# Kernel tuning notes

Measured on AMD Instinct MI355X. Metric: run time of the kernel, lower is better.

Reference implementation:

```python
import jax, jax.numpy as jnp
import numpy as np

GRID_SHAPE = (32, 32)
TEMPERATURE = 1.0


def setup_inputs() -> dict:
    key = jax.random.key(0)
    k1, k2 = jax.random.split(key)
    x = jax.random.normal(k1, (16384, 1024), dtype=jnp.float32)
    som_weights = jax.random.normal(k2, (*GRID_SHAPE, 1024), dtype=jnp.float32) * 0.05
    return {"x": x, "som_weights": som_weights}


def reference(x, som_weights):
    # x: [B, D]; som_weights: [G1, G2, D]
    B, D = x.shape
    g1, g2 = GRID_SHAPE
    w_flat = som_weights.reshape(g1 * g2, D)  # [N, D]
    x_sq = jnp.sum(x * x, axis=-1, keepdims=True)          # [B, 1]
    w_sq = jnp.sum(w_flat * w_flat, axis=-1)[None, :]       # [1, N]
    d2 = x_sq - 2.0 * (x @ w_flat.T) + w_sq                 # [B, N]
    logits = (-d2 / TEMPERATURE).reshape(B, g1, g2)         # [B, G1, G2]
    # per-dimension softmax along each spatial axis, combined multiplicatively
    s1 = jax.nn.softmax(logits, axis=1)
    s2 = jax.nn.softmax(logits, axis=2)
    combined = s1 * s2
    combined = combined / (jnp.sum(combined, axis=(1, 2), keepdims=True) + 1e-8)
    # soft reconstruction: weighted sum over grid of codebook vectors
    recon = jnp.einsum('bn,nd->bd', combined.reshape(B, g1 * g2), w_flat)
    return recon
```

## Files before the change

### kernel.cpp

```cpp
#include <hip/hip_runtime.h>
#include <hip/hip_bf16.h>

static constexpr int BATCH = 16384;
static constexpr int DIM   = 1024;
static constexpr int NN    = 1024;
static constexpr int G     = 32;

typedef _Float16 half8  __attribute__((ext_vector_type(8)));
typedef _Float16 half4v __attribute__((ext_vector_type(4)));
typedef float    f32x4  __attribute__((ext_vector_type(4)));

__global__ __launch_bounds__(256) void transpose_w_kernel(const float* __restrict__ W,
                                                          _Float16* __restrict__ Wh,
                                                          _Float16* __restrict__ WTh) {
    __shared__ _Float16 tile[64][72];
    const int t  = threadIdx.x;
    const int n0 = (blockIdx.x & 15) * 64;
    const int d0 = (blockIdx.x >> 4) * 64;
#pragma unroll
    for (int p = 0; p < 4; ++p) {
        int n = n0 + p * 16 + (t >> 4);
        int d = d0 + (t & 15) * 4;
        float4 v = *(const float4*)(W + (size_t)n * DIM + d);
        half4v h;
        h[0] = (_Float16)v.x; h[1] = (_Float16)v.y;
        h[2] = (_Float16)v.z; h[3] = (_Float16)v.w;
        *(half4v*)(Wh + (size_t)n * DIM + d) = h;
#pragma unroll
        for (int k = 0; k < 4; ++k)
            tile[(t & 15) * 4 + k][p * 16 + (t >> 4)] = h[k];
    }
    __syncthreads();
#pragma unroll
    for (int p = 0; p < 4; ++p) {
        int dp = p * 16 + (t >> 4);
        int nc = (t & 15) * 4;
        half4v hv = *(const half4v*)&tile[dp][nc];
        *(half4v*)(WTh + (size_t)(d0 + dp) * NN + n0 + nc) = hv;
    }
}

__global__ __launch_bounds__(256) void wsq_kernel(const float* __restrict__ W,
                                                  float* __restrict__ wsq) {
    const int n = blockIdx.x;
    const int t = threadIdx.x;
    float4 v = *(const float4*)(W + (size_t)n * DIM + 4 * t);
    float ss = v.x * v.x + v.y * v.y + v.z * v.z + v.w * v.w;
#pragma unroll
    for (int o = 32; o > 0; o >>= 1) ss += __shfl_xor(ss, o, 64);
    __shared__ float red[4];
    if ((t & 63) == 0) red[t >> 6] = ss;
    __syncthreads();
    if (t == 0) wsq[n] = red[0] + red[1] + red[2] + red[3];
}

template <typename AT, int EPI>
__global__ __launch_bounds__(256) void gemm_bt_kernel(const AT* __restrict__ A,
                                                      const _Float16* __restrict__ B,
                                                      float* __restrict__ C,
                                                      const float* __restrict__ wsq,
                                                      int M, int N, int K) {
    constexpr bool AF32 = sizeof(AT) == 4;
    __shared__ __align__(16) AT       As[128 * 64];
    __shared__ __align__(16) _Float16 Bs[128 * 64];

    const int t  = threadIdx.x;
    const int l  = t & 63;
    const int wv = t >> 6;

    const int NT  = N >> 7;
    const int MT  = M >> 7;
    const int lid = blockIdx.x;
    const int xcd = lid & 7;
    const int i0  = lid >> 3;
    const int bn  = (i0 % NT) * 128;
    const int bm  = (xcd * (MT >> 3) + i0 / NT) * 128;

    const int wm = (wv >> 1) * 64;
    const int wn = (wv & 1) * 64;

    auto stage = [&](int k0) {
        if constexpr (AF32) {
#pragma unroll
            for (int j = 0; j < 8; ++j) {
                int rbase = wv * 32 + j * 4;
                int row   = rbase + (l >> 4);
                int c     = (l & 15) ^ (row & 15);
                const float* gA = (const float*)A + (size_t)(bm + row) * K + k0 + c * 4;
                __builtin_amdgcn_global_load_lds(
                    (const __attribute__((address_space(1))) void*)gA,
                    (__attribute__((address_space(3))) void*)((float*)As + rbase * 64),
                    16, 0, 0);
            }
        } else {
#pragma unroll
            for (int j = 0; j < 4; ++j) {
                int rbase = wv * 32 + j * 8;
                int row   = rbase + (l >> 3);
                int c     = (l & 7) ^ (row & 7);
                const _Float16* gA = (const _Float16*)A + (size_t)(bm + row) * K + k0 + c * 8;
                __builtin_amdgcn_global_load_lds(
                    (const __attribute__((address_space(1))) void*)gA,
                    (__attribute__((address_space(3))) void*)((_Float16*)As + rbase * 64),
                    16, 0, 0);
            }
        }
#pragma unroll
        for (int j = 0; j < 4; ++j) {
            int rbase = wv * 32 + j * 8;
            int row   = rbase + (l >> 3);
            int c     = (l & 7) ^ (row & 7);
            const _Float16* gB = B + (size_t)(bn + row) * K + k0 + c * 8;
            __builtin_amdgcn_global_load_lds(
                (const __attribute__((address_space(1))) void*)gB,
                (__attribute__((address_space(3))) void*)(Bs + rbase * 64),
                16, 0, 0);
        }
    };

    f32x4 acc[4][4] = {};
    stage(0);

    for (int kt = 0; kt < K; kt += 64) {
        __syncthreads();
#pragma unroll
        for (int sub = 0; sub < 2; ++sub) {
            half8 af[4], bf[4];
#pragma unroll
            for (int mi = 0; mi < 4; ++mi) {
                if constexpr (AF32) {
                    const float* pa = (const float*)As + (wm + (l & 15) + mi * 16) * 64;
                    int cpair = sub * 8 + (l >> 4) * 2;
                    f32x4 lo = *(const f32x4*)(pa + ((cpair     ) ^ (l & 15)) * 4);
                    f32x4 hi = *(const f32x4*)(pa + ((cpair + 1) ^ (l & 15)) * 4);
#pragma unroll
                    for (int q = 0; q < 4; ++q) {
                        af[mi][q]     = (_Float16)lo[q];
                        af[mi][4 + q] = (_Float16)hi[q];
                    }
                } else {
                    const _Float16* pa = (const _Float16*)As + (wm + (l & 15) + mi * 16) * 64;
                    int c = sub * 4 + (l >> 4);
                    af[mi] = *(const half8*)(pa + (c ^ (l & 7)) * 8);
                }
            }
#pragma unroll
            for (int ni = 0; ni < 4; ++ni) {
                const _Float16* pb = Bs + (wn + (l & 15) + ni * 16) * 64;
                int c = sub * 4 + (l >> 4);
                bf[ni] = *(const half8*)(pb + (c ^ (l & 7)) * 8);
            }
#pragma unroll
            for (int mi = 0; mi < 4; ++mi)
#pragma unroll
                for (int ni = 0; ni < 4; ++ni)
                    acc[mi][ni] = __builtin_amdgcn_mfma_f32_16x16x32_f16(
                        af[mi], bf[ni], acc[mi][ni], 0, 0, 0);
        }
        __syncthreads();
        if (kt + 64 < K) stage(kt + 64);
    }

#pragma unroll
    for (int mi = 0; mi < 4; ++mi) {
        const int rbase = bm + wm + mi * 16 + (l >> 4) * 4;
#pragma unroll
        for (int ni = 0; ni < 4; ++ni) {
            const int col = bn + wn + ni * 16 + (l & 15);
            float wq = (EPI == 1) ? wsq[col] : 0.f;
#pragma unroll
            for (int r = 0; r < 4; ++r) {
                float v = acc[mi][ni][r];
                if (EPI == 1) v = 2.f * v - wq;
                C[(size_t)(rbase + r) * N + col] = v;
            }
        }
    }
}

__global__ __launch_bounds__(256) void softmax_kernel(const float* __restrict__ L,
                                                      _Float16* __restrict__ Ch) {
    const int l  = threadIdx.x & 63;
    const int wv = threadIdx.x >> 6;
    const int b  = blockIdx.x * 4 + wv;

    const f32x4* Lr = (const f32x4*)(L + (size_t)b * NN);
    f32x4 v[4];
#pragma unroll
    for (int i = 0; i < 4; ++i) v[i] = Lr[i * 64 + l];

    float er[4][4], ec[4][4];
    float rinv[4];
#pragma unroll
    for (int i = 0; i < 4; ++i) {
        float m = fmaxf(fmaxf(v[i][0], v[i][1]), fmaxf(v[i][2], v[i][3]));
        m = fmaxf(m, __shfl_xor(m, 1, 64));
        m = fmaxf(m, __shfl_xor(m, 2, 64));
        m = fmaxf(m, __shfl_xor(m, 4, 64));
        float s = 0.f;
#pragma unroll
        for (int j = 0; j < 4; ++j) { er[i][j] = __expf(v[i][j] - m); s += er[i][j]; }
        s += __shfl_xor(s, 1, 64);
        s += __shfl_xor(s, 2, 64);
        s += __shfl_xor(s, 4, 64);
        rinv[i] = 1.f / s;
    }
#pragma unroll
    for (int j = 0; j < 4; ++j) {
        float m = fmaxf(fmaxf(v[0][j], v[1][j]), fmaxf(v[2][j], v[3][j]));
        m = fmaxf(m, __shfl_xor(m, 8, 64));
        m = fmaxf(m, __shfl_xor(m, 16, 64));
        m = fmaxf(m, __shfl_xor(m, 32, 64));
        float s = 0.f;
#pragma unroll
        for (int i = 0; i < 4; ++i) { ec[i][j] = __expf(v[i][j] - m); s += ec[i][j]; }
        s += __shfl_xor(s, 8, 64);
        s += __shfl_xor(s, 16, 64);
        s += __shfl_xor(s, 32, 64);
        float ci = 1.f / s;
#pragma unroll
        for (int i = 0; i < 4; ++i) ec[i][j] *= ci;
    }
    float c[4][4];
    float tot = 0.f;
#pragma unroll
    for (int i = 0; i < 4; ++i)
#pragma unroll
        for (int j = 0; j < 4; ++j) {
            c[i][j] = er[i][j] * rinv[i] * ec[i][j];
            tot += c[i][j];
        }
#pragma unroll
    for (int o = 32; o > 0; o >>= 1) tot += __shfl_xor(tot, o, 64);
    float inv = 1.f / (tot + 1e-8f);
#pragma unroll
    for (int i = 0; i < 4; ++i) {
        half4v h;
#pragma unroll
        for (int j = 0; j < 4; ++j) h[j] = (_Float16)(c[i][j] * inv);
        ((half4v*)(Ch + (size_t)b * NN))[i * 64 + l] = h;
    }
}

extern "C" void kernel_launch(void* const* d_in, const int* in_sizes, int n_in,
                              void* d_out, int out_size, void* d_ws, size_t ws_size,
                              hipStream_t stream) {
    const float* x = (const float*)d_in[0];
    const float* w = (const float*)d_in[1];
    float* out = (float*)d_out;

    char* ws = (char*)d_ws;
    size_t off = 0;
    _Float16* ch  = (_Float16*)(ws + off); off += (size_t)BATCH * NN * 2;
    float*    L   = (float*)   (ws + off); off += (size_t)BATCH * NN * 4;
    _Float16* wh  = (_Float16*)(ws + off); off += (size_t)NN * DIM * 2;
    _Float16* wth = (_Float16*)(ws + off); off += (size_t)DIM * NN * 2;
    float*    wsq = (float*)   (ws + off); off += (size_t)NN * 4;

    transpose_w_kernel<<<256, 256, 0, stream>>>(w, wh, wth);
    wsq_kernel<<<NN, 256, 0, stream>>>(w, wsq);
    gemm_bt_kernel<float, 1><<<(BATCH / 128) * (NN / 128), 256, 0, stream>>>(
        x, wh, L, wsq, BATCH, NN, DIM);
    softmax_kernel<<<BATCH / 4, 256, 0, stream>>>(L, ch);
    gemm_bt_kernel<_Float16, 0><<<(BATCH / 128) * (DIM / 128), 256, 0, stream>>>(
        ch, wth, out, nullptr, BATCH, DIM, NN);
}
```

Before: 245.0 us.

## Pre-convert x to fp16 and double-buffer LDS tiles in GEMM

Adds a kernel that converts x to fp16 into the softmax output workspace, so the first GEMM loads fp16 A tiles instead of fp32 and skips per-fragment conversion. The GEMM now uses two LDS buffers so the next k-tile's async global-to-LDS loads overlap current MFMA work, with one barrier per iteration. This adds an extra pass over x and raises LDS usage, which may reduce occupancy.

Result: faster. 229.1 us (-6.5%).

```diff
diff --git a/kernel.cpp b/kernel.cpp
--- a/kernel.cpp
+++ b/kernel.cpp
@@ -9,6 +9,17 @@
 typedef _Float16 half8  __attribute__((ext_vector_type(8)));
 typedef _Float16 half4v __attribute__((ext_vector_type(4)));
 typedef float    f32x4  __attribute__((ext_vector_type(4)));
+
+__global__ __launch_bounds__(256) void cvt_x_kernel(const float* __restrict__ x,
+                                                    _Float16* __restrict__ xh) {
+    size_t i = ((size_t)blockIdx.x * 256 + threadIdx.x) * 8;
+    f32x4 a = *(const f32x4*)(x + i);
+    f32x4 b = *(const f32x4*)(x + i + 4);
+    half8 h;
+#pragma unroll
+    for (int q = 0; q < 4; ++q) { h[q] = (_Float16)a[q]; h[4 + q] = (_Float16)b[q]; }
+    *(half8*)(xh + i) = h;
+}
 
 __global__ __launch_bounds__(256) void transpose_w_kernel(const float* __restrict__ W,
                                                           _Float16* __restrict__ Wh,
@@ -54,15 +65,14 @@
     if (t == 0) wsq[n] = red[0] + red[1] + red[2] + red[3];
 }
 
-template <typename AT, int EPI>
-__global__ __launch_bounds__(256) void gemm_bt_kernel(const AT* __restrict__ A,
+template <int EPI>
+__global__ __launch_bounds__(256) void gemm_bt_kernel(const _Float16* __restrict__ A,
                                                       const _Float16* __restrict__ B,
                                                       float* __restrict__ C,
                                                       const float* __restrict__ wsq,
                                                       int M, int N, int K) {
-    constexpr bool AF32 = sizeof(AT) == 4;
-    __shared__ __align__(16) AT       As[128 * 64];
-    __shared__ __align__(16) _Float16 Bs[128 * 64];
+    __shared__ __align__(16) _Float16 As[2][128 * 64];
+    __shared__ __align__(16) _Float16 Bs[2][128 * 64];
 
     const int t  = threadIdx.x;
     const int l  = t & 63;
@@ -79,74 +89,44 @@
     const int wm = (wv >> 1) * 64;
     const int wn = (wv & 1) * 64;
 
-    auto stage = [&](int k0) {
-        if constexpr (AF32) {
-#pragma unroll
-            for (int j = 0; j < 8; ++j) {
-                int rbase = wv * 32 + j * 4;
-                int row   = rbase + (l >> 4);
-                int c     = (l & 15) ^ (row & 15);
-                const float* gA = (const float*)A + (size_t)(bm + row) * K + k0 + c * 4;
-                __builtin_amdgcn_global_load_lds(
-                    (const __attribute__((address_space(1))) void*)gA,
-                    (__attribute__((address_space(3))) void*)((float*)As + rbase * 64),
-                    16, 0, 0);
-            }
-        } else {
-#pragma unroll
-            for (int j = 0; j < 4; ++j) {
-                int rbase = wv * 32 + j * 8;
-                int row   = rbase + (l >> 3);
-                int c     = (l & 7) ^ (row & 7);
-                const _Float16* gA = (const _Float16*)A + (size_t)(bm + row) * K + k0 + c * 8;
-                __builtin_amdgcn_global_load_lds(
-                    (const __attribute__((address_space(1))) void*)gA,
-                    (__attribute__((address_space(3))) void*)((_Float16*)As + rbase * 64),
-                    16, 0, 0);
-            }
-        }
+    auto stage = [&](int buf, int k0) {
 #pragma unroll
         for (int j = 0; j < 4; ++j) {
             int rbase = wv * 32 + j * 8;
             int row   = rbase + (l >> 3);
             int c     = (l & 7) ^ (row & 7);
+            const _Float16* gA = A + (size_t)(bm + row) * K + k0 + c * 8;
+            __builtin_amdgcn_global_load_lds(
+                (const __attribute__((address_space(1))) void*)gA,
+                (__attribute__((address_space(3))) void*)(&As[buf][rbase * 64]),
+                16, 0, 0);
             const _Float16* gB = B + (size_t)(bn + row) * K + k0 + c * 8;
             __builtin_amdgcn_global_load_lds(
                 (const __attribute__((address_space(1))) void*)gB,
-                (__attribute__((address_space(3))) void*)(Bs + rbase * 64),
+                (__attribute__((address_space(3))) void*)(&Bs[buf][rbase * 64]),
                 16, 0, 0);
         }
     };
 
     f32x4 acc[4][4] = {};
-    stage(0);
-
+    stage(0, 0);
+    __syncthreads();
+
+    int cur = 0;
     for (int kt = 0; kt < K; kt += 64) {
-        __syncthreads();
+        if (kt + 64 < K) stage(cur ^ 1, kt + 64);
 #pragma unroll
         for (int sub = 0; sub < 2; ++sub) {
             half8 af[4], bf[4];
 #pragma unroll
             for (int mi = 0; mi < 4; ++mi) {
-                if constexpr (AF32) {
-                    const float* pa = (const float*)As + (wm + (l & 15) + mi * 16) * 64;
-                    int cpair = sub * 8 + (l >> 4) * 2;
-                    f32x4 lo = *(const f32x4*)(pa + ((cpair     ) ^ (l & 15)) * 4);
-                    f32x4 hi = *(const f32x4*)(pa + ((cpair + 1) ^ (l & 15)) * 4);
-#pragma unroll
-                    for (int q = 0; q < 4; ++q) {
-                        af[mi][q]     = (_Float16)lo[q];
-                        af[mi][4 + q] = (_Float16)hi[q];
-                    }
-                } else {
-                    const _Float16* pa = (const _Float16*)As + (wm + (l & 15) + mi * 16) * 64;
-                    int c = sub * 4 + (l >> 4);
-                    af[mi] = *(const half8*)(pa + (c ^ (l & 7)) * 8);
-                }
+                const _Float16* pa = &As[cur][(wm + (l & 15) + mi * 16) * 64];
+                int c = sub * 4 + (l >> 4);
+                af[mi] = *(const half8*)(pa + (c ^ (l & 7)) * 8);
             }
 #pragma unroll
             for (int ni = 0; ni < 4; ++ni) {
-                const _Float16* pb = Bs + (wn + (l & 15) + ni * 16) * 64;
+                const _Float16* pb = &Bs[cur][(wn + (l & 15) + ni * 16) * 64];
                 int c = sub * 4 + (l >> 4);
                 bf[ni] = *(const half8*)(pb + (c ^ (l & 7)) * 8);
             }
@@ -158,7 +138,7 @@
                         af[mi], bf[ni], acc[mi][ni], 0, 0, 0);
         }
         __syncthreads();
-        if (kt + 64 < K) stage(kt + 64);
+        cur ^= 1;
     }
 
 #pragma unroll
@@ -257,11 +237,14 @@
     _Float16* wth = (_Float16*)(ws + off); off += (size_t)DIM * NN * 2;
     float*    wsq = (float*)   (ws + off); off += (size_t)NN * 4;
 
+    _Float16* xh = ch;
+
+    cvt_x_kernel<<<(BATCH * DIM) / (256 * 8), 256, 0, stream>>>(x, xh);
     transpose_w_kernel<<<256, 256, 0, stream>>>(w, wh, wth);
     wsq_kernel<<<NN, 256, 0, stream>>>(w, wsq);
-    gemm_bt_kernel<float, 1><<<(BATCH / 128) * (NN / 128), 256, 0, stream>>>(
-        x, wh, L, wsq, BATCH, NN, DIM);
+    gemm_bt_kernel<1><<<(BATCH / 128) * (NN / 128), 256, 0, stream>>>(
+        xh, wh, L, wsq, BATCH, NN, DIM);
     softmax_kernel<<<BATCH / 4, 256, 0, stream>>>(L, ch);
-    gemm_bt_kernel<_Float16, 0><<<(BATCH / 128) * (DIM / 128), 256, 0, stream>>>(
+    gemm_bt_kernel<0><<<(BATCH / 128) * (DIM / 128), 256, 0, stream>>>(
         ch, wth, out, nullptr, BATCH, DIM, NN);
 }
```
